# Performance work log

Measured on AMD Instinct MI355X. Metric: run time of the kernel, lower is better.

The kernel has to match this reference:

```python
import jax, jax.numpy as jnp
import numpy as np

D_MODEL = 512
NUM_HEADS = 8
D_HEAD = 64
BATCH = 2
SEQ = 2048
NEG_BIG = 1.0e10


def setup_inputs() -> dict:
    key = jax.random.key(0)
    k1, k2, k3, k4, k5 = jax.random.split(key, 5)
    scale = D_MODEL ** -0.5
    return {
        "x": jax.random.normal(k1, (BATCH, SEQ, D_MODEL), dtype=jnp.float32),
        "W_Q": jax.random.normal(k2, (NUM_HEADS, D_HEAD, D_MODEL), dtype=jnp.float32) * scale,
        "W_K": jax.random.normal(k3, (NUM_HEADS, D_HEAD, D_MODEL), dtype=jnp.float32) * scale,
        "W_V": jax.random.normal(k4, (NUM_HEADS, D_HEAD, D_MODEL), dtype=jnp.float32) * scale,
        "W_O": jax.random.normal(k5, (D_MODEL, D_HEAD * NUM_HEADS), dtype=jnp.float32) * scale,
    }


def reference(x, W_Q, W_K, W_V, W_O):
    b, n, d = x.shape
    # q,k,v: [b, heads, pos, d_head]
    q = jnp.einsum('ihd,bpd->biph', W_Q, x)
    k = jnp.einsum('ihd,bpd->biph', W_K, x)
    v = jnp.einsum('ihd,bpd->biph', W_V, x)
    # scores: [b, heads, q_pos, k_pos]
    scores = jnp.einsum('biph,biqh->biqp', k, q)
    tril = jnp.tril(jnp.ones((n, n), dtype=scores.dtype))   # keep p <= q
    triu = jnp.triu(jnp.ones((n, n), dtype=scores.dtype))   # buffer 'mask'
    # Faithful to source: tril(scores) - 1e10 * (1 - triu)
    masked = scores * tril - NEG_BIG * (1.0 - triu)
    attn = jax.nn.softmax(masked / (D_HEAD ** 0.5), axis=-1)
    z = jnp.einsum('biph,biqp->biqh', v, attn)               # [b, i, q, h]
    z_flat = jnp.transpose(z, (0, 2, 1, 3)).reshape(b, n, -1)  # [b, q, i*h]
    out = jnp.einsum('df,bqf->bqd', W_O, z_flat)
    return out
```

## Files before the change

kernel.cpp:

```cpp
#include <hip/hip_runtime.h>
#include <stdint.h>

#define BATCH 2
#define SEQ 2048
#define DM 512
#define NH 8
#define DH 64
#define MROWS (BATCH * SEQ)
#define NCHUNK 64
#define CHUNK (SEQ / NCHUNK)

typedef __attribute__((ext_vector_type(8))) short bf16x8;
typedef __attribute__((ext_vector_type(4))) float f32x4;

__device__ __forceinline__ unsigned short f2bf(float f) {
    union { float f; uint32_t u; } x; x.f = f;
    uint32_t r = x.u + 0x7fffu + ((x.u >> 16) & 1u);
    return (unsigned short)(r >> 16);
}
__device__ __forceinline__ float bf2f(unsigned short s) {
    union { uint32_t u; float f; } x; x.u = ((uint32_t)s) << 16;
    return x.f;
}

__device__ __forceinline__ void gl_lds16(const void* g, void* l) {
    __builtin_amdgcn_global_load_lds(
        (const __attribute__((address_space(1))) void*)(uintptr_t)g,
        (__attribute__((address_space(3))) void*)(uint32_t)(uintptr_t)l,
        16, 0, 0);
}

__device__ __forceinline__ uint32_t cvtpk(float a, float b) {
    uint32_t d;
    asm volatile("v_cvt_pk_bf16_f32 %0, %1, %2" : "=v"(d) : "v"(a), "v"(b));
    return d;
}

__global__ __launch_bounds__(256, 2) void proj(
    const float* __restrict__ xf, const float* __restrict__ Wqf,
    const float* __restrict__ Wkf, const float* __restrict__ Wvf,
    float* __restrict__ cA, float* __restrict__ cW,
    unsigned short* __restrict__ V, float* __restrict__ csum)
{
    __shared__ __align__(16) unsigned short S[2 * 256 * 32];
    const int t = threadIdx.x, lane = t & 63, wave = t >> 6;
    const int lr2 = lane >> 2;
    const int csrc = ((lane & 3) ^ ((lane >> 3) & 3)) * 8;
    const int l15 = lane & 15, q = lane >> 4;
    const int bid = blockIdx.x;
    const int wm = wave * 32;

    if (bid < 256) {
        constexpr int TE = 256 * 32;
        const int head = (bid >> 3) & 7;
        const int m0 = (((bid >> 6) << 3) | (bid & 7)) * 128;
        const float* gf[4];
#pragma unroll
        for (int r = 0; r < 4; r++) {
            int g = (r * 4 + wave) * 16 + lr2;
            gf[r] = (g < 128) ? xf + (size_t)(m0 + g) * 512 + csrc
                  : (g < 192) ? Wqf + (size_t)(head * 64 + g - 128) * 512 + csrc
                              : Wkf + (size_t)(head * 64 + g - 192) * 512 + csrc;
        }
        int aoff[2], boff[8];
#pragma unroll
        for (int i = 0; i < 2; i++) {
            int R = wm + i * 16 + l15;
            aoff[i] = R * 32 + ((q ^ ((R >> 1) & 3)) * 8);
        }
#pragma unroll
        for (int j = 0; j < 8; j++) {
            int R = 128 + j * 16 + l15;
            boff[j] = R * 32 + ((q ^ ((R >> 1) & 3)) * 8);
        }
        f32x4 acc[2][8];
#pragma unroll
        for (int i = 0; i < 2; i++)
#pragma unroll
            for (int j = 0; j < 8; j++) { f32x4 z = {0.f,0.f,0.f,0.f}; acc[i][j] = z; }

        float4 RA[4][2], RB[4][2];
        auto load = [&](float4 (&R)[4][2], int tt) {
            const int k0 = tt * 32;
#pragma unroll
            for (int r = 0; r < 4; r++) {
                R[r][0] = *(const float4*)(gf[r] + k0);
                R[r][1] = *(const float4*)(gf[r] + k0 + 4);
            }
        };
        auto cw = [&](float4 (&R)[4][2], int buf) {
#pragma unroll
            for (int r = 0; r < 4; r++) {
                uint4 o;
                o.x = cvtpk(R[r][0].x, R[r][0].y);
                o.y = cvtpk(R[r][0].z, R[r][0].w);
                o.z = cvtpk(R[r][1].x, R[r][1].y);
                o.w = cvtpk(R[r][1].z, R[r][1].w);
                *(uint4*)(S + buf * TE + (r * 4 + wave) * 512 + lane * 8) = o;
            }
        };
        auto compute = [&](int buf) {
            const unsigned short* Sb = S + buf * TE;
            bf16x8 af[2], bfr[8];
#pragma unroll
            for (int i = 0; i < 2; i++) af[i] = *(const bf16x8*)(Sb + aoff[i]);
#pragma unroll
            for (int j = 0; j < 8; j++) bfr[j] = *(const bf16x8*)(Sb + boff[j]);
            __builtin_amdgcn_s_setprio(1);
#pragma unroll
            for (int i = 0; i < 2; i++)
#pragma unroll
                for (int j = 0; j < 8; j++)
                    acc[i][j] = __builtin_amdgcn_mfma_f32_16x16x32_bf16(af[i], bfr[j], acc[i][j], 0, 0, 0);
            __builtin_amdgcn_s_setprio(0);
        };

        load(RA, 0); load(RB, 1);
        asm volatile("s_waitcnt vmcnt(8)" ::: "memory");
        cw(RA, 0);
        asm volatile("s_waitcnt lgkmcnt(0)" ::: "memory");
        __builtin_amdgcn_s_barrier();
        for (int tt = 0; tt < 14; tt += 2) {
            load(RA, tt + 2);
            compute(0);
            asm volatile("s_waitcnt vmcnt(8)" ::: "memory");
            cw(RB, 1);
            asm volatile("s_waitcnt lgkmcnt(0)" ::: "memory");
            __builtin_amdgcn_s_barrier();
            load(RB, tt + 3);
            compute(1);
            asm volatile("s_waitcnt vmcnt(8)" ::: "memory");
            cw(RA, 0);
            asm volatile("s_waitcnt lgkmcnt(0)" ::: "memory");
            __builtin_amdgcn_s_barrier();
        }
        compute(0);
        asm volatile("s_waitcnt vmcnt(0)" ::: "memory");
        cw(RB, 1);
        asm volatile("s_waitcnt lgkmcnt(0)" ::: "memory");
        __builtin_amdgcn_s_barrier();
        compute(1);

#pragma unroll
        for (int i = 0; i < 2; i++)
#pragma unroll
            for (int r = 0; r < 4; r++) {
                float d = 0.f;
#pragma unroll
                for (int j = 0; j < 4; j++) d += acc[i][j][r] * acc[i][j + 4][r];
                d += __shfl_xor(d, 1); d += __shfl_xor(d, 2);
                d += __shfl_xor(d, 4); d += __shfl_xor(d, 8);
                if (l15 == 0) {
                    int row = m0 + wm + i * 16 + (lane >> 4) * 4 + r;
                    int p = row & (SEQ - 1);
                    float dd = d * 0.125f;
                    float M = fmaxf(dd, 0.f);
                    float a = expf(dd - M), e0 = expf(-M);
                    float Z = a + (float)(SEQ - 1 - p) * e0;
                    cA[row * NH + head] = a / Z;
                    cW[row * NH + head] = e0 / Z;
                }
            }
    } else {
        constexpr int TE2 = 192 * 32;
        const int b2 = bid - 256;
        const int head = (b2 >> 3) & 7;
        const int m0 = (((b2 >> 6) << 3) | (b2 & 7)) * 128;
        const int n0 = head * 64;
        const float* gf[3];
#pragma unroll
        for (int r = 0; r < 3; r++) {
            int g = (r * 4 + wave) * 16 + lr2;
            gf[r] = (g < 128) ? xf + (size_t)(m0 + g) * 512 + csrc
                              : Wvf + (size_t)(head * 64 + g - 128) * 512 + csrc;
        }
        int aoff[2], boff[4];
#pragma unroll
        for (int i = 0; i < 2; i++) {
            int R = wm + i * 16 + l15;
            aoff[i] = R * 32 + ((q ^ ((R >> 1) & 3)) * 8);
        }
#pragma unroll
        for (int j = 0; j < 4; j++) {
            int R = 128 + j * 16 + l15;
            boff[j] = R * 32 + ((q ^ ((R >> 1) & 3)) * 8);
        }
        f32x4 acc[2][4];
#pragma unroll
        for (int i = 0; i < 2; i++)
#pragma unroll
            for (int j = 0; j < 4; j++) { f32x4 z = {0.f,0.f,0.f,0.f}; acc[i][j] = z; }

        float4 RA[3][2], RB[3][2];
        auto load = [&](float4 (&R)[3][2], int tt) {
            const int k0 = tt * 32;
#pragma unroll
            for (int r = 0; r < 3; r++) {
                R[r][0] = *(const float4*)(gf[r] + k0);
                R[r][1] = *(const float4*)(gf[r] + k0 + 4);
            }
        };
        auto cw = [&](float4 (&R)[3][2], int buf) {
#pragma unroll
            for (int r = 0; r < 3; r++) {
                uint4 o;
                o.x = cvtpk(R[r][0].x, R[r][0].y);
                o.y = cvtpk(R[r][0].z, R[r][0].w);
                o.z = cvtpk(R[r][1].x, R[r][1].y);
                o.w = cvtpk(R[r][1].z, R[r][1].w);
                *(uint4*)(S + buf * TE2 + (r * 4 + wave) * 512 + lane * 8) = o;
            }
        };
        auto compute = [&](int buf) {
            const unsigned short* Sb = S + buf * TE2;
            bf16x8 af[2], bfr[4];
#pragma unroll
            for (int i = 0; i < 2; i++) af[i] = *(const bf16x8*)(Sb + aoff[i]);
#pragma unroll
            for (int j = 0; j < 4; j++) bfr[j] = *(const bf16x8*)(Sb + boff[j]);
            __builtin_amdgcn_s_setprio(1);
#pragma unroll
            for (int i = 0; i < 2; i++)
#pragma unroll
                for (int j = 0; j < 4; j++)
                    acc[i][j] = __builtin_amdgcn_mfma_f32_16x16x32_bf16(af[i], bfr[j], acc[i][j], 0, 0, 0);
            __builtin_amdgcn_s_setprio(0);
        };

        load(RA, 0); load(RB, 1);
        asm volatile("s_waitcnt vmcnt(6)" ::: "memory");
        cw(RA, 0);
        asm volatile("s_waitcnt lgkmcnt(0)" ::: "memory");
        __builtin_amdgcn_s_barrier();
        for (int tt = 0; tt < 14; tt += 2) {
            load(RA, tt + 2);
            compute(0);
            asm volatile("s_waitcnt vmcnt(6)" ::: "memory");
            cw(RB, 1);
            asm volatile("s_waitcnt lgkmcnt(0)" ::: "memory");
            __builtin_amdgcn_s_barrier();
            load(RB, tt + 3);
            compute(1);
            asm volatile("s_waitcnt vmcnt(6)" ::: "memory");
            cw(RA, 0);
            asm volatile("s_waitcnt lgkmcnt(0)" ::: "memory");
            __builtin_amdgcn_s_barrier();
        }
        compute(0);
        asm volatile("s_waitcnt vmcnt(0)" ::: "memory");
        cw(RB, 1);
        asm volatile("s_waitcnt lgkmcnt(0)" ::: "memory");
        __builtin_amdgcn_s_barrier();
        compute(1);

        const int crow = m0 + wm + (lane >> 4) * 4;
#pragma unroll
        for (int i = 0; i < 2; i++)
#pragma unroll
            for (int j = 0; j < 4; j++)
#pragma unroll
                for (int r = 0; r < 4; r++)
                    V[(size_t)(crow + i * 16 + r) * DM + n0 + j * 16 + l15] = f2bf(acc[i][j][r]);
        float s[4];
#pragma unroll
        for (int j = 0; j < 4; j++) {
            s[j] = 0.f;
#pragma unroll
            for (int i = 0; i < 2; i++)
#pragma unroll
                for (int r = 0; r < 4; r++) s[j] += acc[i][j][r];
            s[j] += __shfl_xor(s[j], 16);
            s[j] += __shfl_xor(s[j], 32);
        }
        if (lane < 16) {
            int bi = (m0 >> 11) * NH + head;
            int chunk = ((m0 & (SEQ - 1)) >> 5) + wave;
#pragma unroll
            for (int j = 0; j < 4; j++)
                csum[(bi * NCHUNK + chunk) * 64 + j * 16 + lane] = s[j];
        }
    }
}

__global__ __launch_bounds__(256) void zbuild(
    const unsigned short* __restrict__ V, const float* __restrict__ csum,
    const float* __restrict__ cA, const float* __restrict__ cW,
    const float4* __restrict__ Wo, ushort4* __restrict__ wob,
    unsigned short* __restrict__ Zb) {
    {
        int idx = blockIdx.x * 256 + threadIdx.x;
        float4 v = Wo[idx];
        ushort4 o; o.x = f2bf(v.x); o.y = f2bf(v.y); o.z = f2bf(v.z); o.w = f2bf(v.w);
        wob[idx] = o;
    }
    int ci = blockIdx.x * 4 + (threadIdx.x >> 6);
    int h = threadIdx.x & 63;
    int c = ci & (NCHUNK - 1), bi = ci >> 6;
    int i = bi & 7, b = bi >> 3;
    float r = 0.f;
#pragma unroll 4
    for (int cc = c + 1; cc < NCHUNK; cc++) r += csum[((bi << 6) + cc) * 64 + h];
#pragma unroll 4
    for (int j = CHUNK - 1; j >= 0; j--) {
        int p = c * CHUNK + j;
        size_t row = (size_t)(b * SEQ + p);
        float v = bf2f(V[row * DM + i * DH + h]);
        float a = cA[row * NH + i], w = cW[row * NH + i];
        Zb[row * DM + i * DH + h] = f2bf(fmaf(a, v, w * r));
        r += v;
    }
}

template<int TM, int TN, int WM, int WN>
__global__ __launch_bounds__(256) void gemm_bt(
    const unsigned short* __restrict__ A, const unsigned short* __restrict__ B,
    float* __restrict__ C, int M, int N, int K)
{
    constexpr int ROWS = TM + TN;
    static_assert(ROWS == 128, "pipeline waits assume 128 staged rows");
    constexpr int MI = WM / 16, NJ = WN / 16;
    constexpr int WAVES_N = TN / WN;
    constexpr int TE = ROWS * 32;
    __shared__ __align__(16) unsigned short S[4 * TE];
    const int t = threadIdx.x, lane = t & 63, wave = t >> 6;
    const int wm = (wave / WAVES_N) * WM, wn = (wave % WAVES_N) * WN;
    const int m0 = blockIdx.x * TM, n0 = blockIdx.y * TN;
    const int lr2 = lane >> 2;
    const int csrc = ((lane & 3) ^ ((lane >> 3) & 3)) * 8;
    const int l15 = lane & 15, q = lane >> 4;

    const unsigned short* gb[2];
#pragma unroll
    for (int r = 0; r < 2; r++) {
        int g = (r * 4 + wave) * 16 + lr2;
        gb[r] = (g < TM) ? A + (size_t)(m0 + g) * K + csrc
                         : B + (size_t)(n0 + g - TM) * K + csrc;
    }
    int aoff[MI], boff[NJ];
#pragma unroll
    for (int i = 0; i < MI; i++) {
        int R = wm + i * 16 + l15;
        aoff[i] = R * 32 + ((q ^ ((R >> 1) & 3)) * 8);
    }
#pragma unroll
    for (int j = 0; j < NJ; j++) {
        int R = TM + wn + j * 16 + l15;
        boff[j] = R * 32 + ((q ^ ((R >> 1) & 3)) * 8);
    }

    f32x4 acc[MI][NJ];
#pragma unroll
    for (int i = 0; i < MI; i++)
#pragma unroll
        for (int j = 0; j < NJ; j++) { f32x4 z = {0.f,0.f,0.f,0.f}; acc[i][j] = z; }

    auto stage = [&](int buf, int tt) {
        const int k0 = tt * 32;
#pragma unroll
        for (int r = 0; r < 2; r++)
            gl_lds16(gb[r] + k0, S + buf * TE + (r * 4 + wave) * 512);
    };
    auto compute = [&](int buf) {
        const unsigned short* Sb = S + buf * TE;
        bf16x8 af[MI], bfr[NJ];
#pragma unroll
        for (int i = 0; i < MI; i++) af[i] = *(const bf16x8*)(Sb + aoff[i]);
#pragma unroll
        for (int j = 0; j < NJ; j++) bfr[j] = *(const bf16x8*)(Sb + boff[j]);
        __builtin_amdgcn_s_setprio(1);
#pragma unroll
        for (int i = 0; i < MI; i++)
#pragma unroll
            for (int j = 0; j < NJ; j++)
                acc[i][j] = __builtin_amdgcn_mfma_f32_16x16x32_bf16(af[i], bfr[j], acc[i][j], 0, 0, 0);
        __builtin_amdgcn_s_setprio(0);
    };

    const int NT = K / 32;
    stage(0, 0); stage(1, 1); stage(2, 2);
    for (int tt = 0; tt < NT - 2; ++tt) {
        asm volatile("s_waitcnt vmcnt(4)" ::: "memory");
        __builtin_amdgcn_s_barrier();
        compute(tt & 3);
        if (tt + 3 < NT) stage((tt + 3) & 3, tt + 3);
    }
    asm volatile("s_waitcnt vmcnt(2)" ::: "memory");
    __builtin_amdgcn_s_barrier();
    compute((NT - 2) & 3);
    asm volatile("s_waitcnt vmcnt(0)" ::: "memory");
    __builtin_amdgcn_s_barrier();
    compute((NT - 1) & 3);

    const int crow = m0 + wm + (lane >> 4) * 4;
    const int ccol = n0 + wn + (lane & 15);
#pragma unroll
    for (int i = 0; i < MI; i++)
#pragma unroll
        for (int j = 0; j < NJ; j++)
#pragma unroll
            for (int r = 0; r < 4; r++)
                C[(size_t)(crow + i * 16 + r) * N + ccol + j * 16] = acc[i][j][r];
}

extern "C" void kernel_launch(void* const* d_in, const int* in_sizes, int n_in,
                              void* d_out, int out_size, void* d_ws, size_t ws_size,
                              hipStream_t stream) {
    const float* x  = (const float*)d_in[0];
    const float* Wq = (const float*)d_in[1];
    const float* Wk = (const float*)d_in[2];
    const float* Wv = (const float*)d_in[3];
    const float* Wo = (const float*)d_in[4];
    float* out = (float*)d_out;
    char* ws = (char*)d_ws;

    unsigned short* wb = (unsigned short*)(ws + 4194304);
    unsigned short* V  = (unsigned short*)(ws + 6291456);
    float* cA = (float*)(ws + 10485760);
    float* cW = (float*)(ws + 10616832);
    float* cs = (float*)(ws + 10747904);
    unsigned short* Zb = (unsigned short*)(ws + 11010048);

    proj<<<512, 256, 0, stream>>>(x, Wq, Wk, Wv, cA, cW, V, cs);
    zbuild<<<256, 256, 0, stream>>>(V, cs, cA, cW, (const float4*)Wo,
                                    (ushort4*)(wb + 786432), Zb);
    gemm_bt<64, 64, 32, 32><<<dim3(64, 8, 1), 256, 0, stream>>>(
        Zb, wb + 786432, out, MROWS, DM, DM);
}
```

Before: 96.04 us.

## Fuse Z construction into output GEMM and move W_O conversion into projection

The separate zbuild kernel is removed. Each zgemm block now builds its own 32-row chunk of Z straight into swizzled LDS from V, the chunk suffix sums and the per-row coefficients, then runs the W_O GEMM against that LDS-resident A operand. The W_O fp32-to-bf16 conversion moves to the tail of the proj kernel. This saves one kernel launch and the global write and read of the Z buffer. In exchange, each of the four column-tile blocks per chunk recomputes the same Z chunk, so Z construction work is redundant.

```diff
diff --git a/kernel.cpp b/kernel.cpp
--- a/kernel.cpp
+++ b/kernel.cpp
@@ -40,7 +40,8 @@
     const float* __restrict__ xf, const float* __restrict__ Wqf,
     const float* __restrict__ Wkf, const float* __restrict__ Wvf,
     float* __restrict__ cA, float* __restrict__ cW,
-    unsigned short* __restrict__ V, float* __restrict__ csum)
+    unsigned short* __restrict__ V, float* __restrict__ csum,
+    const float4* __restrict__ Wo4, ushort4* __restrict__ wob)
 {
     __shared__ __align__(16) unsigned short S[2 * 256 * 32];
     const int t = threadIdx.x, lane = t & 63, wave = t >> 6;
@@ -280,126 +281,129 @@
                 csum[(bi * NCHUNK + chunk) * 64 + j * 16 + lane] = s[j];
         }
     }
-}
-
-__global__ __launch_bounds__(256) void zbuild(
+
+    {
+        int idx = bid * 256 + t;
+        if (idx < 65536) {
+            float4 v = Wo4[idx];
+            ushort4 o; o.x = f2bf(v.x); o.y = f2bf(v.y); o.z = f2bf(v.z); o.w = f2bf(v.w);
+            wob[idx] = o;
+        }
+    }
+}
+
+__global__ __launch_bounds__(256) void zgemm(
     const unsigned short* __restrict__ V, const float* __restrict__ csum,
     const float* __restrict__ cA, const float* __restrict__ cW,
-    const float4* __restrict__ Wo, ushort4* __restrict__ wob,
-    unsigned short* __restrict__ Zb) {
-    {
-        int idx = blockIdx.x * 256 + threadIdx.x;
-        float4 v = Wo[idx];
-        ushort4 o; o.x = f2bf(v.x); o.y = f2bf(v.y); o.z = f2bf(v.z); o.w = f2bf(v.w);
-        wob[idx] = o;
-    }
-    int ci = blockIdx.x * 4 + (threadIdx.x >> 6);
-    int h = threadIdx.x & 63;
-    int c = ci & (NCHUNK - 1), bi = ci >> 6;
-    int i = bi & 7, b = bi >> 3;
-    float r = 0.f;
-#pragma unroll 4
-    for (int cc = c + 1; cc < NCHUNK; cc++) r += csum[((bi << 6) + cc) * 64 + h];
-#pragma unroll 4
-    for (int j = CHUNK - 1; j >= 0; j--) {
-        int p = c * CHUNK + j;
-        size_t row = (size_t)(b * SEQ + p);
-        float v = bf2f(V[row * DM + i * DH + h]);
-        float a = cA[row * NH + i], w = cW[row * NH + i];
-        Zb[row * DM + i * DH + h] = f2bf(fmaf(a, v, w * r));
-        r += v;
-    }
-}
-
-template<int TM, int TN, int WM, int WN>
-__global__ __launch_bounds__(256) void gemm_bt(
-    const unsigned short* __restrict__ A, const unsigned short* __restrict__ B,
-    float* __restrict__ C, int M, int N, int K)
+    const unsigned short* __restrict__ wob, float* __restrict__ out)
 {
-    constexpr int ROWS = TM + TN;
-    static_assert(ROWS == 128, "pipeline waits assume 128 staged rows");
-    constexpr int MI = WM / 16, NJ = WN / 16;
-    constexpr int WAVES_N = TN / WN;
-    constexpr int TE = ROWS * 32;
-    __shared__ __align__(16) unsigned short S[4 * TE];
+    __shared__ __align__(16) unsigned short S[16384 + 4 * 4096];
+    unsigned short* Z = S;
+    unsigned short* SB = S + 16384;
     const int t = threadIdx.x, lane = t & 63, wave = t >> 6;
-    const int wm = (wave / WAVES_N) * WM, wn = (wave % WAVES_N) * WN;
-    const int m0 = blockIdx.x * TM, n0 = blockIdx.y * TN;
+    const int bid = blockIdx.x;
+    const int qdx = bid & 3, cidx = bid >> 2;
+    const int b = cidx >> 6, c = cidx & 63;
+    const int n0 = qdx * 128;
     const int lr2 = lane >> 2;
     const int csrc = ((lane & 3) ^ ((lane >> 3) & 3)) * 8;
     const int l15 = lane & 15, q = lane >> 4;
 
+    {
+        const int c0 = t * 2;
+        const int head = c0 >> 6, h0 = c0 & 63;
+        float r0 = 0.f, r1 = 0.f;
+        const float* cb = csum + (size_t)((b * NH + head) * NCHUNK) * 64;
+#pragma unroll 4
+        for (int cc = c + 1; cc < NCHUNK; cc++) {
+            float2 s2 = *(const float2*)(cb + cc * 64 + h0);
+            r0 += s2.x; r1 += s2.y;
+        }
+        const size_t rbase = (size_t)(b * SEQ + c * CHUNK);
+#pragma unroll 8
+        for (int j = CHUNK - 1; j >= 0; j--) {
+            size_t row = rbase + j;
+            uint32_t vv = *(const uint32_t*)(V + row * DM + c0);
+            float v0 = bf2f((unsigned short)(vv & 0xffff));
+            float v1 = bf2f((unsigned short)(vv >> 16));
+            float a = cA[row * NH + head], w = cW[row * NH + head];
+            float z0 = fmaf(a, v0, w * r0);
+            float z1 = fmaf(a, v1, w * r1);
+            *(uint32_t*)(Z + j * 512 + (((c0 >> 3) ^ (j & 7)) * 8) + (c0 & 7)) =
+                cvtpk(z0, z1);
+            r0 += v0; r1 += v1;
+        }
+    }
+    __syncthreads();
+
+    constexpr int TE = 4096;
     const unsigned short* gb[2];
 #pragma unroll
     for (int r = 0; r < 2; r++) {
         int g = (r * 4 + wave) * 16 + lr2;
-        gb[r] = (g < TM) ? A + (size_t)(m0 + g) * K + csrc
-                         : B + (size_t)(n0 + g - TM) * K + csrc;
-    }
-    int aoff[MI], boff[NJ];
-#pragma unroll
-    for (int i = 0; i < MI; i++) {
-        int R = wm + i * 16 + l15;
-        aoff[i] = R * 32 + ((q ^ ((R >> 1) & 3)) * 8);
-    }
-#pragma unroll
-    for (int j = 0; j < NJ; j++) {
-        int R = TM + wn + j * 16 + l15;
+        gb[r] = wob + (size_t)(n0 + g) * 512 + csrc;
+    }
+    int boff[2];
+#pragma unroll
+    for (int j = 0; j < 2; j++) {
+        int R = wave * 32 + j * 16 + l15;
         boff[j] = R * 32 + ((q ^ ((R >> 1) & 3)) * 8);
     }
-
-    f32x4 acc[MI][NJ];
-#pragma unroll
-    for (int i = 0; i < MI; i++)
-#pragma unroll
-        for (int j = 0; j < NJ; j++) { f32x4 z = {0.f,0.f,0.f,0.f}; acc[i][j] = z; }
+    f32x4 acc[2][2];
+#pragma unroll
+    for (int i = 0; i < 2; i++)
+#pragma unroll
+        for (int j = 0; j < 2; j++) { f32x4 z = {0.f,0.f,0.f,0.f}; acc[i][j] = z; }
 
     auto stage = [&](int buf, int tt) {
         const int k0 = tt * 32;
 #pragma unroll
         for (int r = 0; r < 2; r++)
-            gl_lds16(gb[r] + k0, S + buf * TE + (r * 4 + wave) * 512);
+            gl_lds16(gb[r] + k0, SB + buf * TE + (r * 4 + wave) * 512);
     };
-    auto compute = [&](int buf) {
-        const unsigned short* Sb = S + buf * TE;
-        bf16x8 af[MI], bfr[NJ];
-#pragma unroll
-        for (int i = 0; i < MI; i++) af[i] = *(const bf16x8*)(Sb + aoff[i]);
-#pragma unroll
-        for (int j = 0; j < NJ; j++) bfr[j] = *(const bf16x8*)(Sb + boff[j]);
+    auto compute = [&](int buf, int tt) {
+        const unsigned short* Sb = SB + buf * TE;
+        bf16x8 af[2], bfr[2];
+        const int cc = tt * 4 + q;
+#pragma unroll
+        for (int i = 0; i < 2; i++) {
+            int R = i * 16 + l15;
+            af[i] = *(const bf16x8*)(Z + R * 512 + ((cc ^ (R & 7)) * 8));
+        }
+#pragma unroll
+        for (int j = 0; j < 2; j++) bfr[j] = *(const bf16x8*)(Sb + boff[j]);
         __builtin_amdgcn_s_setprio(1);
 #pragma unroll
-        for (int i = 0; i < MI; i++)
-#pragma unroll
-            for (int j = 0; j < NJ; j++)
+        for (int i = 0; i < 2; i++)
+#pragma unroll
+            for (int j = 0; j < 2; j++)
                 acc[i][j] = __builtin_amdgcn_mfma_f32_16x16x32_bf16(af[i], bfr[j], acc[i][j], 0, 0, 0);
         __builtin_amdgcn_s_setprio(0);
     };
 
-    const int NT = K / 32;
     stage(0, 0); stage(1, 1); stage(2, 2);
-    for (int tt = 0; tt < NT - 2; ++tt) {
+    for (int tt = 0; tt < 14; ++tt) {
         asm volatile("s_waitcnt vmcnt(4)" ::: "memory");
         __builtin_amdgcn_s_barrier();
-        compute(tt & 3);
-        if (tt + 3 < NT) stage((tt + 3) & 3, tt + 3);
+        compute(tt & 3, tt);
+        if (tt + 3 < 16) stage((tt + 3) & 3, tt + 3);
     }
     asm volatile("s_waitcnt vmcnt(2)" ::: "memory");
     __builtin_amdgcn_s_barrier();
-    compute((NT - 2) & 3);
+    compute(2, 14);
     asm volatile("s_waitcnt vmcnt(0)" ::: "memory");
     __builtin_amdgcn_s_barrier();
-    compute((NT - 1) & 3);
-
-    const int crow = m0 + wm + (lane >> 4) * 4;
-    const int ccol = n0 + wn + (lane & 15);
-#pragma unroll
-    for (int i = 0; i < MI; i++)
-#pragma unroll
-        for (int j = 0; j < NJ; j++)
+    compute(3, 15);
+
+    const int crow = cidx * 32 + (lane >> 4) * 4;
+    const int ccol = n0 + wave * 32 + l15;
+#pragma unroll
+    for (int i = 0; i < 2; i++)
+#pragma unroll
+        for (int j = 0; j < 2; j++)
 #pragma unroll
             for (int r = 0; r < 4; r++)
-                C[(size_t)(crow + i * 16 + r) * N + ccol + j * 16] = acc[i][j][r];
+                out[(size_t)(crow + i * 16 + r) * DM + ccol + j * 16] = acc[i][j][r];
 }
 
 extern "C" void kernel_launch(void* const* d_in, const int* in_sizes, int n_in,
@@ -413,16 +417,13 @@
     float* out = (float*)d_out;
     char* ws = (char*)d_ws;
 
-    unsigned short* wb = (unsigned short*)(ws + 4194304);
-    unsigned short* V  = (unsigned short*)(ws + 6291456);
+    unsigned short* wob = (unsigned short*)(ws + 4194304) + 786432;
+    unsigned short* V   = (unsigned short*)(ws + 6291456);
     float* cA = (float*)(ws + 10485760);
     float* cW = (float*)(ws + 10616832);
     float* cs = (float*)(ws + 10747904);
-    unsigned short* Zb = (unsigned short*)(ws + 11010048);
-
-    proj<<<512, 256, 0, stream>>>(x, Wq, Wk, Wv, cA, cW, V, cs);
-    zbuild<<<256, 256, 0, stream>>>(V, cs, cA, cW, (const float4*)Wo,
-                                    (ushort4*)(wb + 786432), Zb);
-    gemm_bt<64, 64, 32, 32><<<dim3(64, 8, 1), 256, 0, stream>>>(
-        Zb, wb + 786432, out, MROWS, DM, DM);
-}
+
+    proj<<<512, 256, 0, stream>>>(x, Wq, Wk, Wv, cA, cW, V, cs,
+                                  (const float4*)Wo, (ushort4*)wob);
+    zgemm<<<512, 256, 0, stream>>>(V, cs, cA, cW, wob, out);
+}
```

New measurement: 97.03 us. No clear change (+1.0%).
